# Optimization experiments

Measured on AMD Instinct MI355X. Metric: run time of the kernel, lower is better.

## Reference

```python
import jax, jax.numpy as jnp
import numpy as np

M = 4096       # number of graphs (rows of h)
N = 262144     # total nodes across the batch
DH = 128       # d_h
DX = 128       # d_x

def setup_inputs() -> dict:
    key = jax.random.key(0)
    k1, k2, k3, k4 = jax.random.split(key, 4)
    h = jax.random.normal(k1, (M, DH), dtype=jnp.float32)
    x = jax.random.normal(k2, (N, DX), dtype=jnp.float32)
    a = 0.001 * jax.random.uniform(k3, (DH, DX), dtype=jnp.float32)  # nn.Parameter init
    segment_ids = jnp.sort(jax.random.randint(k4, (N,), 0, M))  # ragged graph membership
    return {"h": h, "x": x, "a": a, "segment_ids": segment_ids}

def reference(h, x, a, segment_ids):
    # proj[g] = h[g] @ a, broadcast to nodes via segment_ids (== repeat_interleave by batch_num_nodes)
    proj = h @ a                                    # (m, d_x)
    s = jnp.sum(x * proj[segment_ids], axis=1)      # (n,) per-node score
    # segment softmax (max for stability, exp, sum)
    smax = jax.ops.segment_max(s, segment_ids, num_segments=M)
    smax = jnp.where(jnp.isfinite(smax), smax, 0.0)  # guard empty segments
    e = jnp.exp(s - smax[segment_ids])              # (n,)
    z = jax.ops.segment_sum(e, segment_ids, num_segments=M)
    att = e / z[segment_ids]                        # (n,) normalized attention
    # weighted sum of node features per graph
    return jax.ops.segment_sum(att[:, None] * x, segment_ids, num_segments=M)  # (m, d_x)
```

## Files before the change

### kernel.cpp

```cpp
#include <hip/hip_runtime.h>
#include <hip/hip_bf16.h>
#include <math.h>

#define MSEG  4096
#define NNODE 262144
#define DDIM  128
#define CHUNK 64
#define PROJ_ROWS 16

template<int CTRL>
__device__ __forceinline__ float dpp_zero(float v) {
    return __int_as_float(__builtin_amdgcn_update_dpp(
        0, __float_as_int(v), CTRL, 0xF, 0xF, true));
}
template<int CTRL>
__device__ __forceinline__ float dpp_self(float v) {
    int iv = __float_as_int(v);
    return __int_as_float(__builtin_amdgcn_update_dpp(iv, iv, CTRL, 0xF, 0xF, false));
}
__device__ __forceinline__ float rdlane(float v, int lane_const) {
    return __int_as_float(__builtin_amdgcn_readlane(__float_as_int(v), lane_const));
}
__device__ __forceinline__ float row16_sum(float v) {
    v += dpp_zero<0x111>(v);
    v += dpp_zero<0x112>(v);
    v += dpp_zero<0x114>(v);
    v += dpp_zero<0x118>(v);
    return v;
}
__device__ __forceinline__ float wave_sum64(float v) {
    v = row16_sum(v);
    return (rdlane(v, 15) + rdlane(v, 31)) + (rdlane(v, 47) + rdlane(v, 63));
}
__device__ __forceinline__ float wave_max64(float v) {
    v = fmaxf(v, dpp_self<0x111>(v));
    v = fmaxf(v, dpp_self<0x112>(v));
    v = fmaxf(v, dpp_self<0x114>(v));
    v = fmaxf(v, dpp_self<0x118>(v));
    return fmaxf(fmaxf(rdlane(v, 15), rdlane(v, 31)),
                 fmaxf(rdlane(v, 47), rdlane(v, 63)));
}

__global__ __launch_bounds__(256) void seg_starts_kernel(
    const int* __restrict__ seg, int* __restrict__ starts)
{
    int i = blockIdx.x * blockDim.x + threadIdx.x;
    if (i >= NNODE) return;
    int s = seg[i];
    int prev = (i == 0) ? -1 : seg[i - 1];
    for (int g = prev + 1; g <= s; ++g) starts[g] = i;
    if (i == NNODE - 1)
        for (int g = s + 1; g <= MSEG; ++g) starts[g] = NNODE;
}

__global__ __launch_bounds__(256) void proj_kernel(
    const float* __restrict__ h, const float* __restrict__ a,
    float* __restrict__ proj)
{
    __shared__ __align__(16) float a_lds[DDIM * DDIM];
    __shared__ __align__(16) float h_lds[PROJ_ROWS * DDIM];
    const int tid = threadIdx.x;
    const int g0  = blockIdx.x * PROJ_ROWS;

    const float4* a4  = (const float4*)a;
    float4*       al4 = (float4*)a_lds;
    #pragma unroll
    for (int j = 0; j < (DDIM * DDIM / 4) / 256; ++j)
        al4[j * 256 + tid] = a4[j * 256 + tid];
    const float4* h4  = (const float4*)(h + (size_t)g0 * DDIM);
    float4*       hl4 = (float4*)h_lds;
    #pragma unroll
    for (int j = 0; j < (PROJ_ROWS * DDIM / 4) / 256; ++j)
        hl4[j * 256 + tid] = h4[j * 256 + tid];
    __syncthreads();

    const int dp = tid & 63;
    const int rh = tid >> 6;
    const float2* al2 = (const float2*)a_lds;
    #pragma unroll
    for (int rr = 0; rr < PROJ_ROWS / 4; ++rr) {
        const int r = rh * (PROJ_ROWS / 4) + rr;
        float2 p = make_float2(0.f, 0.f);
        #pragma unroll 8
        for (int k = 0; k < DDIM; ++k) {
            const float  hv = h_lds[r * DDIM + k];
            const float2 av = al2[k * 64 + dp];
            p.x += hv * av.x;
            p.y += hv * av.y;
        }
        ((float2*)(proj + (size_t)(g0 + r) * DDIM))[dp] = p;
    }
}

__global__ __launch_bounds__(256) void attn_seg_kernel(
    const float* __restrict__ x,
    const float* __restrict__ proj,
    const int*   __restrict__ starts,
    float*       __restrict__ out)
{
    __shared__ float s_lds[CHUNK];
    __shared__ float e_lds[CHUNK];
    __shared__ __align__(16) float4 racc4[512];

    const int g   = blockIdx.x;
    const int tid = threadIdx.x;
    const int l   = tid & 15;
    const int r   = tid >> 4;
    const int L   = tid & 63;

    const int start = starts[g];
    const int end   = starts[g + 1];

    if (start >= end) {
        if (tid < 32)
            ((float4*)out)[(size_t)g * 32 + tid] = make_float4(0.f, 0.f, 0.f, 0.f);
        return;
    }

    const float4* __restrict__ x4p = (const float4*)x;
    const float4 pj0 = ((const float4*)proj)[(size_t)g * 32 + 2 * l];
    const float4 pj1 = ((const float4*)proj)[(size_t)g * 32 + 2 * l + 1];

    float m_run = -INFINITY;
    float l_run = 0.f;
    float4 acc0 = make_float4(0.f, 0.f, 0.f, 0.f);
    float4 acc1 = make_float4(0.f, 0.f, 0.f, 0.f);

    int cs = start;
    int n_c = min(CHUNK, end - start);
    float4 xv0[4], xv1[4];
    #pragma unroll
    for (int p = 0; p < 4; ++p) {
        const int i = p * 16 + r;
        xv0[p] = make_float4(0.f, 0.f, 0.f, 0.f);
        xv1[p] = make_float4(0.f, 0.f, 0.f, 0.f);
        if (i < n_c) {
            const size_t base = (size_t)(cs + i) * 32 + 2 * l;
            xv0[p] = x4p[base];
            xv1[p] = x4p[base + 1];
        }
    }

    while (true) {
        #pragma unroll
        for (int p = 0; p < 4; ++p) {
            const int i = p * 16 + r;
            float ps = xv0[p].x * pj0.x + xv0[p].y * pj0.y
                     + xv0[p].z * pj0.z + xv0[p].w * pj0.w
                     + xv1[p].x * pj1.x + xv1[p].y * pj1.y
                     + xv1[p].z * pj1.z + xv1[p].w * pj1.w;
            ps = row16_sum(ps);
            if (l == 15 && i < n_c) s_lds[i] = ps;
        }
        __syncthreads();

        const float sv = (L < n_c) ? s_lds[L] : -INFINITY;
        const float m_new = fmaxf(m_run, wave_max64(sv));
        const float ev = (L < n_c) ? __expf(sv - m_new) : 0.f;
        const float lc = wave_sum64(ev);
        if (tid < 64) e_lds[tid] = ev;
        const float alpha = __expf(m_run - m_new);
        l_run = l_run * alpha + lc;
        m_run = m_new;
        acc0.x *= alpha; acc0.y *= alpha; acc0.z *= alpha; acc0.w *= alpha;
        acc1.x *= alpha; acc1.y *= alpha; acc1.z *= alpha; acc1.w *= alpha;
        __syncthreads();

        #pragma unroll
        for (int p = 0; p < 4; ++p) {
            const float e = e_lds[p * 16 + r];
            acc0.x += e * xv0[p].x; acc0.y += e * xv0[p].y;
            acc0.z += e * xv0[p].z; acc0.w += e * xv0[p].w;
            acc1.x += e * xv1[p].x; acc1.y += e * xv1[p].y;
            acc1.z += e * xv1[p].z; acc1.w += e * xv1[p].w;
        }

        cs += CHUNK;
        if (cs >= end) break;
        n_c = min(CHUNK, end - cs);
        #pragma unroll
        for (int p = 0; p < 4; ++p) {
            const int i = p * 16 + r;
            xv0[p] = make_float4(0.f, 0.f, 0.f, 0.f);
            xv1[p] = make_float4(0.f, 0.f, 0.f, 0.f);
            if (i < n_c) {
                const size_t base = (size_t)(cs + i) * 32 + 2 * l;
                xv0[p] = x4p[base];
                xv1[p] = x4p[base + 1];
            }
        }
        __syncthreads();
    }

    racc4[r * 32 + 2 * l]     = acc0;
    racc4[r * 32 + 2 * l + 1] = acc1;
    __syncthreads();
    if (tid < 32) {
        float4 s = racc4[tid];
        #pragma unroll
        for (int rr = 1; rr < 16; ++rr) {
            const float4 t = racc4[rr * 32 + tid];
            s.x += t.x; s.y += t.y; s.z += t.z; s.w += t.w;
        }
        const float inv = 1.f / l_run;
        ((float4*)out)[(size_t)g * 32 + tid] =
            make_float4(s.x * inv, s.y * inv, s.z * inv, s.w * inv);
    }
}

extern "C" void kernel_launch(void* const* d_in, const int* in_sizes, int n_in,
                              void* d_out, int out_size, void* d_ws, size_t ws_size,
                              hipStream_t stream) {
    const float* h   = (const float*)d_in[0];
    const float* x   = (const float*)d_in[1];
    const float* a   = (const float*)d_in[2];
    const int*   seg = (const int*)  d_in[3];
    float* out = (float*)d_out;

    int*   starts = (int*)d_ws;
    float* proj   = (float*)((char*)d_ws + 32768);

    seg_starts_kernel<<<(NNODE + 255) / 256, 256, 0, stream>>>(seg, starts);
    proj_kernel<<<MSEG / PROJ_ROWS, 256, 0, stream>>>(h, a, proj);
    attn_seg_kernel<<<MSEG, 256, 0, stream>>>(x, proj, starts, out);
}
```

Measured before the change: 209.5 us.

## Map one wavefront per segment and drop LDS/barriers from attention kernel

Each 64-lane wavefront now owns a whole segment (four segments per block), processing 16 nodes per chunk with shuffle-based reductions instead of LDS staging and block barriers. The online softmax now rescales lazily, only when the running max jumps by more than a threshold. The cross-row accumulator reduction also moves from LDS to register shuffles. The goal is to remove synchronization and LDS traffic, at the cost of fewer loads in flight per segment and possible load imbalance between waves.

```diff
diff --git a/kernel.cpp b/kernel.cpp
--- a/kernel.cpp
+++ b/kernel.cpp
@@ -1,45 +1,12 @@
 #include <hip/hip_runtime.h>
-#include <hip/hip_bf16.h>
 #include <math.h>
 
 #define MSEG  4096
 #define NNODE 262144
 #define DDIM  128
-#define CHUNK 64
+#define CH    16
+#define SEG_PER_BLK 4
 #define PROJ_ROWS 16
-
-template<int CTRL>
-__device__ __forceinline__ float dpp_zero(float v) {
-    return __int_as_float(__builtin_amdgcn_update_dpp(
-        0, __float_as_int(v), CTRL, 0xF, 0xF, true));
-}
-template<int CTRL>
-__device__ __forceinline__ float dpp_self(float v) {
-    int iv = __float_as_int(v);
-    return __int_as_float(__builtin_amdgcn_update_dpp(iv, iv, CTRL, 0xF, 0xF, false));
-}
-__device__ __forceinline__ float rdlane(float v, int lane_const) {
-    return __int_as_float(__builtin_amdgcn_readlane(__float_as_int(v), lane_const));
-}
-__device__ __forceinline__ float row16_sum(float v) {
-    v += dpp_zero<0x111>(v);
-    v += dpp_zero<0x112>(v);
-    v += dpp_zero<0x114>(v);
-    v += dpp_zero<0x118>(v);
-    return v;
-}
-__device__ __forceinline__ float wave_sum64(float v) {
-    v = row16_sum(v);
-    return (rdlane(v, 15) + rdlane(v, 31)) + (rdlane(v, 47) + rdlane(v, 63));
-}
-__device__ __forceinline__ float wave_max64(float v) {
-    v = fmaxf(v, dpp_self<0x111>(v));
-    v = fmaxf(v, dpp_self<0x112>(v));
-    v = fmaxf(v, dpp_self<0x114>(v));
-    v = fmaxf(v, dpp_self<0x118>(v));
-    return fmaxf(fmaxf(rdlane(v, 15), rdlane(v, 31)),
-                 fmaxf(rdlane(v, 47), rdlane(v, 63)));
-}
 
 __global__ __launch_bounds__(256) void seg_starts_kernel(
     const int* __restrict__ seg, int* __restrict__ starts)
@@ -98,22 +65,21 @@
     const int*   __restrict__ starts,
     float*       __restrict__ out)
 {
-    __shared__ float s_lds[CHUNK];
-    __shared__ float e_lds[CHUNK];
-    __shared__ __align__(16) float4 racc4[512];
-
-    const int g   = blockIdx.x;
     const int tid = threadIdx.x;
-    const int l   = tid & 15;
-    const int r   = tid >> 4;
+    const int g   = blockIdx.x * SEG_PER_BLK + (tid >> 6);
     const int L   = tid & 63;
+    const int l   = L & 15;
+    const int r   = L >> 4;
 
     const int start = starts[g];
     const int end   = starts[g + 1];
+    float4* out4 = (float4*)out;
 
     if (start >= end) {
-        if (tid < 32)
-            ((float4*)out)[(size_t)g * 32 + tid] = make_float4(0.f, 0.f, 0.f, 0.f);
+        if (r == 0) {
+            out4[(size_t)g * 32 + 2 * l]     = make_float4(0.f, 0.f, 0.f, 0.f);
+            out4[(size_t)g * 32 + 2 * l + 1] = make_float4(0.f, 0.f, 0.f, 0.f);
+        }
         return;
     }
 
@@ -126,12 +92,12 @@
     float4 acc0 = make_float4(0.f, 0.f, 0.f, 0.f);
     float4 acc1 = make_float4(0.f, 0.f, 0.f, 0.f);
 
-    int cs = start;
-    int n_c = min(CHUNK, end - start);
+    int cs  = start;
+    int n_c = min(CH, end - cs);
     float4 xv0[4], xv1[4];
     #pragma unroll
     for (int p = 0; p < 4; ++p) {
-        const int i = p * 16 + r;
+        const int i = p * 4 + r;
         xv0[p] = make_float4(0.f, 0.f, 0.f, 0.f);
         xv1[p] = make_float4(0.f, 0.f, 0.f, 0.f);
         if (i < n_c) {
@@ -142,45 +108,50 @@
     }
 
     while (true) {
+        float sc[4];
         #pragma unroll
         for (int p = 0; p < 4; ++p) {
-            const int i = p * 16 + r;
             float ps = xv0[p].x * pj0.x + xv0[p].y * pj0.y
                      + xv0[p].z * pj0.z + xv0[p].w * pj0.w
                      + xv1[p].x * pj1.x + xv1[p].y * pj1.y
                      + xv1[p].z * pj1.z + xv1[p].w * pj1.w;
-            ps = row16_sum(ps);
-            if (l == 15 && i < n_c) s_lds[i] = ps;
+            ps += __shfl_xor(ps, 1);
+            ps += __shfl_xor(ps, 2);
+            ps += __shfl_xor(ps, 4);
+            ps += __shfl_xor(ps, 8);
+            sc[p] = (p * 4 + r < n_c) ? ps : -INFINITY;
         }
-        __syncthreads();
-
-        const float sv = (L < n_c) ? s_lds[L] : -INFINITY;
-        const float m_new = fmaxf(m_run, wave_max64(sv));
-        const float ev = (L < n_c) ? __expf(sv - m_new) : 0.f;
-        const float lc = wave_sum64(ev);
-        if (tid < 64) e_lds[tid] = ev;
-        const float alpha = __expf(m_run - m_new);
-        l_run = l_run * alpha + lc;
-        m_run = m_new;
-        acc0.x *= alpha; acc0.y *= alpha; acc0.z *= alpha; acc0.w *= alpha;
-        acc1.x *= alpha; acc1.y *= alpha; acc1.z *= alpha; acc1.w *= alpha;
-        __syncthreads();
-
+        float mc = fmaxf(fmaxf(sc[0], sc[1]), fmaxf(sc[2], sc[3]));
+        mc = fmaxf(mc, __shfl_xor(mc, 16));
+        mc = fmaxf(mc, __shfl_xor(mc, 32));
+        if (mc - m_run > 30.f) {
+            const float alpha = __expf(m_run - mc);
+            l_run *= alpha;
+            acc0.x *= alpha; acc0.y *= alpha; acc0.z *= alpha; acc0.w *= alpha;
+            acc1.x *= alpha; acc1.y *= alpha; acc1.z *= alpha; acc1.w *= alpha;
+            m_run = mc;
+        }
+        float lsum = 0.f;
         #pragma unroll
         for (int p = 0; p < 4; ++p) {
-            const float e = e_lds[p * 16 + r];
+            const bool valid = (p * 4 + r < n_c);
+            const float e = valid ? __expf(sc[p] - m_run) : 0.f;
+            lsum += e;
             acc0.x += e * xv0[p].x; acc0.y += e * xv0[p].y;
             acc0.z += e * xv0[p].z; acc0.w += e * xv0[p].w;
             acc1.x += e * xv1[p].x; acc1.y += e * xv1[p].y;
             acc1.z += e * xv1[p].z; acc1.w += e * xv1[p].w;
         }
+        lsum += __shfl_xor(lsum, 16);
+        lsum += __shfl_xor(lsum, 32);
+        l_run += lsum;
 
-        cs += CHUNK;
+        cs += CH;
         if (cs >= end) break;
-        n_c = min(CHUNK, end - cs);
+        n_c = min(CH, end - cs);
         #pragma unroll
         for (int p = 0; p < 4; ++p) {
-            const int i = p * 16 + r;
+            const int i = p * 4 + r;
             xv0[p] = make_float4(0.f, 0.f, 0.f, 0.f);
             xv1[p] = make_float4(0.f, 0.f, 0.f, 0.f);
             if (i < n_c) {
@@ -189,22 +160,23 @@
                 xv1[p] = x4p[base + 1];
             }
         }
-        __syncthreads();
     }
 
-    racc4[r * 32 + 2 * l]     = acc0;
-    racc4[r * 32 + 2 * l + 1] = acc1;
-    __syncthreads();
-    if (tid < 32) {
-        float4 s = racc4[tid];
-        #pragma unroll
-        for (int rr = 1; rr < 16; ++rr) {
-            const float4 t = racc4[rr * 32 + tid];
-            s.x += t.x; s.y += t.y; s.z += t.z; s.w += t.w;
-        }
+    acc0.x += __shfl_xor(acc0.x, 16); acc0.y += __shfl_xor(acc0.y, 16);
+    acc0.z += __shfl_xor(acc0.z, 16); acc0.w += __shfl_xor(acc0.w, 16);
+    acc1.x += __shfl_xor(acc1.x, 16); acc1.y += __shfl_xor(acc1.y, 16);
+    acc1.z += __shfl_xor(acc1.z, 16); acc1.w += __shfl_xor(acc1.w, 16);
+    acc0.x += __shfl_xor(acc0.x, 32); acc0.y += __shfl_xor(acc0.y, 32);
+    acc0.z += __shfl_xor(acc0.z, 32); acc0.w += __shfl_xor(acc0.w, 32);
+    acc1.x += __shfl_xor(acc1.x, 32); acc1.y += __shfl_xor(acc1.y, 32);
+    acc1.z += __shfl_xor(acc1.z, 32); acc1.w += __shfl_xor(acc1.w, 32);
+
+    if (r == 0) {
         const float inv = 1.f / l_run;
-        ((float4*)out)[(size_t)g * 32 + tid] =
-            make_float4(s.x * inv, s.y * inv, s.z * inv, s.w * inv);
+        out4[(size_t)g * 32 + 2 * l] =
+            make_float4(acc0.x * inv, acc0.y * inv, acc0.z * inv, acc0.w * inv);
+        out4[(size_t)g * 32 + 2 * l + 1] =
+            make_float4(acc1.x * inv, acc1.y * inv, acc1.z * inv, acc1.w * inv);
     }
 }
 
@@ -222,5 +194,5 @@
 
     seg_starts_kernel<<<(NNODE + 255) / 256, 256, 0, stream>>>(seg, starts);
     proj_kernel<<<MSEG / PROJ_ROWS, 256, 0, stream>>>(h, a, proj);
-    attn_seg_kernel<<<MSEG, 256, 0, stream>>>(x, proj, starts, out);
+    attn_seg_kernel<<<MSEG / SEG_PER_BLK, 256, 0, stream>>>(x, proj, starts, out);
 }
```

Result: no change. 212.7 us (+1.6%).
